# Kernel optimization log

Measured on AMD Instinct MI355X. Metric: run time of the kernel, lower is better.

The kernel has to match this reference:

```python
import jax, jax.numpy as jnp
import numpy as np

B, C, N, T = 8, 128, 512, 12
H = 4


def setup_inputs() -> dict:
    key = jax.random.key(0)
    k1, k2, k3 = jax.random.split(key, 3)
    scale = 1.0 / np.sqrt(C)
    seq = jax.random.normal(k1, (B, C, N, T), dtype=jnp.float32)
    W1 = jax.random.normal(k2, (C, C), dtype=jnp.float32) * scale  # conv1 1x1 weight [out,in]
    W2 = jax.random.normal(k3, (C, C), dtype=jnp.float32) * scale  # conv2 1x1 weight [out,in]
    return {"seq": seq, "W1": W1, "W2": W2}


def reference(seq, W1, W2):
    b, c, n, t = seq.shape
    c4 = c // H
    # 1x1 convs == channel-mixing GEMMs
    f1 = jnp.einsum('oc,bcnt->bont', W1, seq).reshape(b, c4, H, n, t)  # [b,c4,h,n,t]
    f2 = jnp.einsum('oc,bcnt->bont', W2, seq).reshape(b, c4, H, n, t)  # [b,c4,h,n,t]
    # einsum 'bnclm,bcqlm->bnqlm' after the permutes == contract over c4,
    # keep per-(t,h) outer product over nodes
    logits = jnp.einsum('bchnt,bchqt->bnqth', f1, f2)  # [b,n,q,t,h]
    logits = jnp.transpose(logits, (0, 3, 1, 2, 4))     # [b,t,n,q,h]
    return jnp.mean(jax.nn.sigmoid(logits), axis=-1)    # [b,t,n,q]
```

## Files before the change

### kernel.cpp

```cpp
#include <hip/hip_runtime.h>
#include <hip/hip_bf16.h>

#define BB 8
#define CC 128
#define NN 512
#define TT 12
#define HH 4
#define C4 32

typedef float f32x4 __attribute__((ext_vector_type(4)));
typedef __bf16 bf16x8 __attribute__((ext_vector_type(8)));

__global__ __launch_bounds__(256) void wtrans_k(const float* __restrict__ W1,
                                                const float* __restrict__ W2,
                                                float* __restrict__ Wt) {
    int idx = blockIdx.x * 256 + threadIdx.x;
    int sel = idx >> 14;
    int r   = idx & 16383;
    int o = r >> 7, c = r & 127;
    const float* W = sel ? W2 : W1;
    Wt[sel * 16384 + c * 128 + o] = W[r];
}

__global__ __launch_bounds__(256) void conv_k(const float* __restrict__ seq,
                                              const float* __restrict__ Wt,
                                              __hip_bfloat16* __restrict__ F1,
                                              __hip_bfloat16* __restrict__ F2) {
    __shared__ float S[CC][64];

    int bid = blockIdx.x;
    int xcd = bid & 7, g = bid >> 3;
    int t   = g % TT;
    int b   = g / TT;
    int n0  = xcd * 64;
    int slice = b * TT + t;

    int tid = threadIdx.x;
    int n   = tid & 63;
    int og  = __builtin_amdgcn_readfirstlane(tid >> 6);

    for (int idx = tid; idx < CC * 64; idx += 256) {
        int c = idx >> 6, nn = idx & 63;
        S[c][nn] = seq[((size_t)(b * CC + c) * NN + (n0 + nn)) * TT + t];
    }
    __syncthreads();

    for (int conv = 0; conv < 2; ++conv) {
        const float* Wv = Wt + conv * 16384 + og * 32;

        float acc[4][8];
#pragma unroll
        for (int h = 0; h < 4; ++h)
#pragma unroll
            for (int j = 0; j < 8; ++j) acc[h][j] = 0.0f;

#pragma unroll 2
        for (int c = 0; c < CC; ++c) {
            float wv[32];
#pragma unroll
            for (int i = 0; i < 32; ++i) wv[i] = Wv[c * 128 + i];
            float s = S[c][n];
#pragma unroll
            for (int h = 0; h < 4; ++h)
#pragma unroll
                for (int j = 0; j < 8; ++j)
                    acc[h][j] = fmaf(wv[4 * j + h], s, acc[h][j]);
        }

        __hip_bfloat16* Fg = conv ? F2 : F1;
#pragma unroll
        for (int h = 0; h < 4; ++h) {
            bf16x8 v;
#pragma unroll
            for (int j = 0; j < 8; ++j) v[j] = (__bf16)acc[h][j];
            *(bf16x8*)&Fg[((size_t)(slice * HH + h) * NN + (n0 + n)) * C4 + og * 8] = v;
        }
    }
}

__global__ __launch_bounds__(256) void att_k(const __hip_bfloat16* __restrict__ F1,
                                             const __hip_bfloat16* __restrict__ F2,
                                             float* __restrict__ out) {
    int bid = blockIdx.x;
    int xcd = bid & 7, g = bid >> 3;
    int tile = g & 63, sg = g >> 6;
    int slice = sg * 8 + xcd;
    int ti = tile >> 3, tj = tile & 7;
    int n0 = ti * 64, q0 = tj * 64;

    int tid = threadIdx.x;
    int w = tid >> 6, l = tid & 63;
    int wr = w >> 1, wc = w & 1;
    int nw = n0 + wr * 32, qw = q0 + wc * 32;
    int lr = l & 15, lg = l >> 4;

    const __hip_bfloat16* F1s = F1 + (size_t)slice * HH * NN * C4;
    const __hip_bfloat16* F2s = F2 + (size_t)slice * HH * NN * C4;

    f32x4 oacc[2][2];
#pragma unroll
    for (int i = 0; i < 2; ++i)
#pragma unroll
        for (int j = 0; j < 2; ++j) oacc[i][j] = (f32x4){0.f, 0.f, 0.f, 0.f};

#pragma unroll
    for (int h = 0; h < HH; ++h) {
        const __hip_bfloat16* f1h = F1s + h * NN * C4;
        const __hip_bfloat16* f2h = F2s + h * NN * C4;
        bf16x8 a0 = *(const bf16x8*)(f1h + (nw + lr) * C4 + 8 * lg);
        bf16x8 a1 = *(const bf16x8*)(f1h + (nw + 16 + lr) * C4 + 8 * lg);
        bf16x8 b0 = *(const bf16x8*)(f2h + (qw + lr) * C4 + 8 * lg);
        bf16x8 b1 = *(const bf16x8*)(f2h + (qw + 16 + lr) * C4 + 8 * lg);
        f32x4 z = {0.f, 0.f, 0.f, 0.f};
        f32x4 l00 = __builtin_amdgcn_mfma_f32_16x16x32_bf16(a0, b0, z, 0, 0, 0);
        f32x4 l01 = __builtin_amdgcn_mfma_f32_16x16x32_bf16(a0, b1, z, 0, 0, 0);
        f32x4 l10 = __builtin_amdgcn_mfma_f32_16x16x32_bf16(a1, b0, z, 0, 0, 0);
        f32x4 l11 = __builtin_amdgcn_mfma_f32_16x16x32_bf16(a1, b1, z, 0, 0, 0);
#pragma unroll
        for (int r = 0; r < 4; ++r) {
            oacc[0][0][r] += __builtin_amdgcn_rcpf(1.0f + __expf(-l00[r]));
            oacc[0][1][r] += __builtin_amdgcn_rcpf(1.0f + __expf(-l01[r]));
            oacc[1][0][r] += __builtin_amdgcn_rcpf(1.0f + __expf(-l10[r]));
            oacc[1][1][r] += __builtin_amdgcn_rcpf(1.0f + __expf(-l11[r]));
        }
    }

    float* outs = out + (size_t)slice * NN * NN;
#pragma unroll
    for (int i = 0; i < 2; ++i) {
#pragma unroll
        for (int j = 0; j < 2; ++j) {
#pragma unroll
            for (int r = 0; r < 4; ++r) {
                int nn = nw + i * 16 + 4 * lg + r;
                int q  = qw + j * 16 + lr;
                outs[nn * NN + q] = 0.25f * oacc[i][j][r];
            }
        }
    }
}

extern "C" void kernel_launch(void* const* d_in, const int* in_sizes, int n_in,
                              void* d_out, int out_size, void* d_ws, size_t ws_size,
                              hipStream_t stream) {
    const float* seq = (const float*)d_in[0];
    const float* W1  = (const float*)d_in[1];
    const float* W2  = (const float*)d_in[2];
    float* out = (float*)d_out;

    float* Wt = (float*)d_ws;
    __hip_bfloat16* F1 = (__hip_bfloat16*)((char*)d_ws + 2 * 16384 * sizeof(float));
    __hip_bfloat16* F2 = F1 + (size_t)96 * HH * NN * C4;

    wtrans_k<<<128, 256, 0, stream>>>(W1, W2, Wt);
    conv_k<<<768, 256, 0, stream>>>(seq, Wt, F1, F2);
    att_k<<<6144, 256, 0, stream>>>(F1, F2, out);
}
```

Before: 208.6 us.

## Split conv output channels across two blocks and fuse both convs, dropping LDS staging

The conv kernel now launches twice as many blocks, each handling half of the output channels (16 per wave instead of 32), so there is more parallelism and fewer accumulator registers per thread. Both convolutions are computed in one pass over input channels, so each seq value is read once for W1 and W2. The shared-memory staging and barrier are replaced by direct strided global loads of seq. The trade-off is that each seq element is now loaded by two blocks, through uncoalesced stride-T accesses, and the stores to F1 and F2 are narrower.

```diff
diff --git a/kernel.cpp b/kernel.cpp
--- a/kernel.cpp
+++ b/kernel.cpp
@@ -10,6 +10,7 @@
 
 typedef float f32x4 __attribute__((ext_vector_type(4)));
 typedef __bf16 bf16x8 __attribute__((ext_vector_type(8)));
+typedef __bf16 bf16x4 __attribute__((ext_vector_type(4)));
 
 __global__ __launch_bounds__(256) void wtrans_k(const float* __restrict__ W1,
                                                 const float* __restrict__ W2,
@@ -26,55 +27,49 @@
                                               const float* __restrict__ Wt,
                                               __hip_bfloat16* __restrict__ F1,
                                               __hip_bfloat16* __restrict__ F2) {
-    __shared__ float S[CC][64];
-
     int bid = blockIdx.x;
-    int xcd = bid & 7, g = bid >> 3;
-    int t   = g % TT;
-    int b   = g / TT;
+    int xcd = bid & 7;
+    int g   = bid >> 3;
+    int oh  = g & 1;
+    int gg  = g >> 1;
+    int t   = gg % TT;
+    int b   = gg / TT;
     int n0  = xcd * 64;
     int slice = b * TT + t;
 
     int tid = threadIdx.x;
     int n   = tid & 63;
-    int og  = __builtin_amdgcn_readfirstlane(tid >> 6);
+    int og16 = __builtin_amdgcn_readfirstlane(oh * 4 + (tid >> 6));
 
-    for (int idx = tid; idx < CC * 64; idx += 256) {
-        int c = idx >> 6, nn = idx & 63;
-        S[c][nn] = seq[((size_t)(b * CC + c) * NN + (n0 + nn)) * TT + t];
-    }
-    __syncthreads();
+    const float* W1v = Wt + og16 * 16;
+    const float* W2v = Wt + 16384 + og16 * 16;
+    const float* sp  = seq + ((size_t)b * CC * NN + (size_t)(n0 + n)) * TT + t;
 
-    for (int conv = 0; conv < 2; ++conv) {
-        const float* Wv = Wt + conv * 16384 + og * 32;
-
-        float acc[4][8];
+    float acc1[16], acc2[16];
 #pragma unroll
-        for (int h = 0; h < 4; ++h)
-#pragma unroll
-            for (int j = 0; j < 8; ++j) acc[h][j] = 0.0f;
+    for (int m = 0; m < 16; ++m) { acc1[m] = 0.0f; acc2[m] = 0.0f; }
 
 #pragma unroll 2
-        for (int c = 0; c < CC; ++c) {
-            float wv[32];
+    for (int c = 0; c < CC; ++c) {
+        float s = sp[(size_t)c * NN * TT];
 #pragma unroll
-            for (int i = 0; i < 32; ++i) wv[i] = Wv[c * 128 + i];
-            float s = S[c][n];
+        for (int m = 0; m < 16; ++m) {
+            acc1[m] = fmaf(W1v[c * 128 + m], s, acc1[m]);
+            acc2[m] = fmaf(W2v[c * 128 + m], s, acc2[m]);
+        }
+    }
+
 #pragma unroll
-            for (int h = 0; h < 4; ++h)
+    for (int h = 0; h < 4; ++h) {
+        bf16x4 v1, v2;
 #pragma unroll
-                for (int j = 0; j < 8; ++j)
-                    acc[h][j] = fmaf(wv[4 * j + h], s, acc[h][j]);
+        for (int j = 0; j < 4; ++j) {
+            v1[j] = (__bf16)acc1[j * 4 + h];
+            v2[j] = (__bf16)acc2[j * 4 + h];
         }
-
-        __hip_bfloat16* Fg = conv ? F2 : F1;
-#pragma unroll
-        for (int h = 0; h < 4; ++h) {
-            bf16x8 v;
-#pragma unroll
-            for (int j = 0; j < 8; ++j) v[j] = (__bf16)acc[h][j];
-            *(bf16x8*)&Fg[((size_t)(slice * HH + h) * NN + (n0 + n)) * C4 + og * 8] = v;
-        }
+        size_t off = ((size_t)(slice * HH + h) * NN + (n0 + n)) * C4 + og16 * 4;
+        *(bf16x4*)&F1[off] = v1;
+        *(bf16x4*)&F2[off] = v2;
     }
 }
 
@@ -153,6 +148,6 @@
     __hip_bfloat16* F2 = F1 + (size_t)96 * HH * NN * C4;
 
     wtrans_k<<<128, 256, 0, stream>>>(W1, W2, Wt);
-    conv_k<<<768, 256, 0, stream>>>(seq, Wt, F1, F2);
+    conv_k<<<1536, 256, 0, stream>>>(seq, Wt, F1, F2);
     att_k<<<6144, 256, 0, stream>>>(F1, F2, out);
 }
```

After: 212.2 us. Within noise of the previous version (+1.7%).
